# Optimization experiments

Hardware: AMD Instinct MI355X
Metric: run time of the kernel (lower is better)

## Reference

```python
import jax, jax.numpy as jnp
import numpy as np

PAA_SIZE = 64  # init_kwargs paa_size
GAF_TYPE = 'GADF'  # init_kwargs GAF_type


def setup_inputs() -> dict:
    key = jax.random.key(0)
    x = jax.random.uniform(key, (256, 4096, 32), dtype=jnp.float32)
    return {"x": x}


def reference(x):
    # x: [B, T, C]
    B, T, C = x.shape
    # --- rescale: per-sample, per-channel min-max over time axis -> [0, 1]
    x_min = jnp.min(x, axis=1, keepdims=True)
    x_max = jnp.max(x, axis=1, keepdims=True)
    r = (x - x_min) / (x_max - x_min)            # [B, T, C]
    # --- PAA: strided mean over bins of length size = T // paa_size
    size = T // PAA_SIZE
    p = r[:, : PAA_SIZE * size].reshape(B, PAA_SIZE, size, C).sum(axis=2) / size  # [B, P, C]
    # --- GAF construction
    y = jnp.sqrt(1.0 - p * p)                    # [B, P, C]
    if GAF_TYPE == 'GASF':
        # out[b,i,j,c] = x_i x_j - y_i y_j (symmetric)
        out = jnp.einsum('bic,bjc->bijc', p, p) - jnp.einsum('bic,bjc->bijc', y, y)
    else:  # 'GADF'
        # original: -transpose(y x^T - x y^T) => out[b,i,j,c] = y_i x_j - x_i y_j
        out = jnp.einsum('bic,bjc->bijc', y, p) - jnp.einsum('bic,bjc->bijc', p, y)
    return out  # [B, paa_size, paa_size, C]
```

## Files before the change

kernel.cpp:

```cpp
#include <hip/hip_runtime.h>
#include <math.h>

#define BB   256
#define TT   4096
#define CC   32
#define PP   64
#define PSTR 33

__device__ __forceinline__ float4 f4min(float4 a, float4 b) {
    return make_float4(fminf(a.x,b.x), fminf(a.y,b.y), fminf(a.z,b.z), fminf(a.w,b.w));
}
__device__ __forceinline__ float4 f4max(float4 a, float4 b) {
    return make_float4(fmaxf(a.x,b.x), fmaxf(a.y,b.y), fmaxf(a.z,b.z), fmaxf(a.w,b.w));
}
__device__ __forceinline__ void f4add(float4& a, float4 v) {
    a.x += v.x; a.y += v.y; a.z += v.z; a.w += v.w;
}
__device__ __forceinline__ float4 shflxor4(float4 v, int m) {
    return make_float4(__shfl_xor(v.x, m), __shfl_xor(v.y, m),
                       __shfl_xor(v.z, m), __shfl_xor(v.w, m));
}

__global__ __launch_bounds__(1024, 4) void gaf_kernel(const float* __restrict__ x,
                                                      float* __restrict__ out) {
    __shared__ float sp[PP * PSTR];
    __shared__ float sy[PP * PSTR];
    __shared__ float redmin[16 * CC];
    __shared__ float redmax[16 * CC];

    const int tid  = threadIdx.x;
    const int lane = tid & 63;
    const int wave = tid >> 6;
    const int cg   = lane & 7;
    const int b    = blockIdx.x;

    const float4* xw = (const float4*)x + (size_t)b * (TT * CC / 4) + wave * 2048 + lane;

    const float FBIG = 3.402823466e+38f;
    float4 mn = make_float4(FBIG, FBIG, FBIG, FBIG);
    float4 mx = make_float4(-FBIG, -FBIG, -FBIG, -FBIG);
    float4 acc[4];
    #pragma unroll
    for (int g = 0; g < 4; ++g) acc[g] = make_float4(0.f, 0.f, 0.f, 0.f);

    #pragma unroll
    for (int g = 0; g < 4; ++g) {
        float4 buf[8];
        #pragma unroll
        for (int u = 0; u < 8; ++u) buf[u] = xw[(g * 8 + u) * 64];
        #pragma unroll
        for (int u = 0; u < 8; ++u) {
            mn = f4min(mn, buf[u]); mx = f4max(mx, buf[u]); f4add(acc[g], buf[u]);
        }
    }

    #pragma unroll
    for (int m = 8; m <= 32; m <<= 1) {
        mn = f4min(mn, shflxor4(mn, m));
        mx = f4max(mx, shflxor4(mx, m));
        #pragma unroll
        for (int g = 0; g < 4; ++g) f4add(acc[g], shflxor4(acc[g], m));
    }

    if (lane < 8) {
        *(float4*)&redmin[wave * CC + cg * 4] = mn;
        *(float4*)&redmax[wave * CC + cg * 4] = mx;
    }
    __syncthreads();

    float4 gmn = *(const float4*)&redmin[0 * CC + cg * 4];
    float4 gmx = *(const float4*)&redmax[0 * CC + cg * 4];
    #pragma unroll
    for (int w = 1; w < 16; ++w) {
        gmn = f4min(gmn, *(const float4*)&redmin[w * CC + cg * 4]);
        gmx = f4max(gmx, *(const float4*)&redmax[w * CC + cg * 4]);
    }

    float4 inv;
    inv.x = 1.0f / (gmx.x - gmn.x);  inv.y = 1.0f / (gmx.y - gmn.y);
    inv.z = 1.0f / (gmx.z - gmn.z);  inv.w = 1.0f / (gmx.w - gmn.w);
    const float s64 = 1.0f / 64.0f;

    if (lane < 8) {
        #pragma unroll
        for (int g = 0; g < 4; ++g) {
            float4 p, y;
            p.x = (acc[g].x * s64 - gmn.x) * inv.x;  p.y = (acc[g].y * s64 - gmn.y) * inv.y;
            p.z = (acc[g].z * s64 - gmn.z) * inv.z;  p.w = (acc[g].w * s64 - gmn.w) * inv.w;
            y.x = sqrtf(fmaxf(1.f - p.x * p.x, 0.f));  y.y = sqrtf(fmaxf(1.f - p.y * p.y, 0.f));
            y.z = sqrtf(fmaxf(1.f - p.z * p.z, 0.f));  y.w = sqrtf(fmaxf(1.f - p.w * p.w, 0.f));
            const int s = wave * 4 + g;
            *(float4*)&sp[s * PSTR + cg * 4] = p;
            *(float4*)&sy[s * PSTR + cg * 4] = y;
        }
    }
    __syncthreads();

    const int jrow = lane >> 3;
    float4 pj[8], yj[8];
    #pragma unroll
    for (int jc = 0; jc < 8; ++jc) {
        const int j = jc * 8 + jrow;
        pj[jc] = *(const float4*)&sp[j * PSTR + cg * 4];
        yj[jc] = *(const float4*)&sy[j * PSTR + cg * 4];
    }

    float4* ob = (float4*)out + (size_t)b * (PP * PP * CC / 4) + wave * 2048 + lane;

    #pragma unroll
    for (int ii = 0; ii < 4; ++ii) {
        const int i = wave * 4 + ii;
        const float4 pi = *(const float4*)&sp[i * PSTR + cg * 4];
        const float4 yi = *(const float4*)&sy[i * PSTR + cg * 4];
        #pragma unroll
        for (int jc = 0; jc < 8; ++jc) {
            float4 r;
            r.x = yi.x * pj[jc].x - pi.x * yj[jc].x;
            r.y = yi.y * pj[jc].y - pi.y * yj[jc].y;
            r.z = yi.z * pj[jc].z - pi.z * yj[jc].z;
            r.w = yi.w * pj[jc].w - pi.w * yj[jc].w;
            ob[ii * 512 + jc * 64] = r;
        }
    }
}

extern "C" void kernel_launch(void* const* d_in, const int* in_sizes, int n_in,
                              void* d_out, int out_size, void* d_ws, size_t ws_size,
                              hipStream_t stream) {
    const float* x = (const float*)d_in[0];
    float* out = (float*)d_out;
    gaf_kernel<<<BB, 1024, 0, stream>>>(x, out);
}
```

Before: 231.0 us.

## Split GAF into stats and outer-product kernels with more blocks

Replaces the single 256-block fused kernel with two launches. The first computes per-segment sums and partial min/max across 2048 blocks and writes them to workspace. The second uses 1024 blocks to finish the reduction, build p/y, and write output with nontemporal stores. The aim is better occupancy of the GPU's compute units than one block per batch allows. The cost is a second launch and a small workspace round trip, and the old fused kernel is kept as a fallback when workspace is too small.

```diff
diff --git a/kernel.cpp b/kernel.cpp
--- a/kernel.cpp
+++ b/kernel.cpp
@@ -1,5 +1,6 @@
 #include <hip/hip_runtime.h>
 #include <math.h>
+
 
 #define BB   256
 #define TT   4096
@@ -7,6 +8,13 @@
 #define PP   64
 #define PSTR 33
 
+typedef float f32x4 __attribute__((ext_vector_type(4)));
+
+#define SEG_FLOATS  (BB * PP * CC)
+#define MM_FLOATS   (BB * 32 * CC)
+#define WS_FLOATS   (SEG_FLOATS + 2 * MM_FLOATS)
+#define WS_BYTES    (WS_FLOATS * 4)
+
 __device__ __forceinline__ float4 f4min(float4 a, float4 b) {
     return make_float4(fminf(a.x,b.x), fminf(a.y,b.y), fminf(a.z,b.z), fminf(a.w,b.w));
 }
@@ -20,9 +28,139 @@
     return make_float4(__shfl_xor(v.x, m), __shfl_xor(v.y, m),
                        __shfl_xor(v.z, m), __shfl_xor(v.w, m));
 }
-
-__global__ __launch_bounds__(1024, 4) void gaf_kernel(const float* __restrict__ x,
-                                                      float* __restrict__ out) {
+__device__ __forceinline__ void ntstore4(float4* dst, float4 v) {
+    f32x4 t; t.x = v.x; t.y = v.y; t.z = v.z; t.w = v.w;
+    __builtin_nontemporal_store(t, (f32x4*)dst);
+}
+
+__global__ __launch_bounds__(256, 8) void gaf_stats(const float* __restrict__ x,
+                                                    float* __restrict__ ws) {
+    const int tid  = threadIdx.x;
+    const int lane = tid & 63;
+    const int wave = tid >> 6;
+    const int cg   = lane & 7;
+    const int blk  = blockIdx.x;
+    const int b    = blk >> 3;
+    const int ch   = blk & 7;
+
+    const float4* base = (const float4*)x + (size_t)b * (TT * CC / 4)
+                         + ch * 4096 + wave * 1024 + lane;
+
+    const float FBIG = 3.402823466e+38f;
+    float4 mn = make_float4(FBIG, FBIG, FBIG, FBIG);
+    float4 mx = make_float4(-FBIG, -FBIG, -FBIG, -FBIG);
+    float4 acc0 = make_float4(0.f, 0.f, 0.f, 0.f);
+    float4 acc1 = make_float4(0.f, 0.f, 0.f, 0.f);
+
+    float4 buf[8];
+    #pragma unroll
+    for (int u = 0; u < 8; ++u) buf[u] = base[u * 64];
+    #pragma unroll
+    for (int u = 0; u < 8; ++u) { mn = f4min(mn, buf[u]); mx = f4max(mx, buf[u]); f4add(acc0, buf[u]); }
+    #pragma unroll
+    for (int u = 0; u < 8; ++u) buf[u] = base[(8 + u) * 64];
+    #pragma unroll
+    for (int u = 0; u < 8; ++u) { mn = f4min(mn, buf[u]); mx = f4max(mx, buf[u]); f4add(acc1, buf[u]); }
+
+    #pragma unroll
+    for (int m = 8; m <= 32; m <<= 1) {
+        mn = f4min(mn, shflxor4(mn, m));
+        mx = f4max(mx, shflxor4(mx, m));
+        f4add(acc0, shflxor4(acc0, m));
+        f4add(acc1, shflxor4(acc1, m));
+    }
+
+    if (lane < 8) {
+        const int s0 = ch * 8 + wave * 2;
+        *(float4*)&ws[(size_t)b * (PP * CC) + s0 * CC + cg * 4]       = acc0;
+        *(float4*)&ws[(size_t)b * (PP * CC) + (s0 + 1) * CC + cg * 4] = acc1;
+        const int k = ch * 4 + wave;
+        *(float4*)&ws[SEG_FLOATS             + (size_t)b * (32 * CC) + k * CC + cg * 4] = mn;
+        *(float4*)&ws[SEG_FLOATS + MM_FLOATS + (size_t)b * (32 * CC) + k * CC + cg * 4] = mx;
+    }
+}
+
+__global__ __launch_bounds__(256, 4) void gaf_outer(const float* __restrict__ ws,
+                                                    float* __restrict__ out) {
+    __shared__ float sp[PP * PSTR];
+    __shared__ float sy[PP * PSTR];
+    __shared__ float4 lmn[32];
+    __shared__ float4 lmx[32];
+
+    const int tid  = threadIdx.x;
+    const int lane = tid & 63;
+    const int wave = tid >> 6;
+    const int cg   = lane & 7;
+    const int blk  = blockIdx.x;
+    const int b    = blk >> 2;
+    const int i0   = (blk & 3) * 16;
+
+    {
+        const int k = wave * 8 + (lane >> 3);
+        float4 mnk = *(const float4*)&ws[SEG_FLOATS             + (size_t)b * (32 * CC) + k * CC + cg * 4];
+        float4 mxk = *(const float4*)&ws[SEG_FLOATS + MM_FLOATS + (size_t)b * (32 * CC) + k * CC + cg * 4];
+        #pragma unroll
+        for (int m = 8; m <= 32; m <<= 1) {
+            mnk = f4min(mnk, shflxor4(mnk, m));
+            mxk = f4max(mxk, shflxor4(mxk, m));
+        }
+        if (lane < 8) { lmn[wave * 8 + cg] = mnk; lmx[wave * 8 + cg] = mxk; }
+    }
+    __syncthreads();
+
+    {
+        const int cq = tid & 7;
+        float4 mnf = f4min(f4min(lmn[cq], lmn[8 + cq]), f4min(lmn[16 + cq], lmn[24 + cq]));
+        float4 mxf = f4max(f4max(lmx[cq], lmx[8 + cq]), f4max(lmx[16 + cq], lmx[24 + cq]));
+        float4 inv;
+        inv.x = 1.0f / (mxf.x - mnf.x);  inv.y = 1.0f / (mxf.y - mnf.y);
+        inv.z = 1.0f / (mxf.z - mnf.z);  inv.w = 1.0f / (mxf.w - mnf.w);
+        const float s64 = 1.0f / 64.0f;
+        #pragma unroll
+        for (int h = 0; h < 2; ++h) {
+            const int s = (tid >> 3) + h * 32;
+            float4 sum = *(const float4*)&ws[(size_t)b * (PP * CC) + s * CC + cq * 4];
+            float4 p, y;
+            p.x = (sum.x * s64 - mnf.x) * inv.x;  p.y = (sum.y * s64 - mnf.y) * inv.y;
+            p.z = (sum.z * s64 - mnf.z) * inv.z;  p.w = (sum.w * s64 - mnf.w) * inv.w;
+            y.x = sqrtf(fmaxf(1.f - p.x * p.x, 0.f));  y.y = sqrtf(fmaxf(1.f - p.y * p.y, 0.f));
+            y.z = sqrtf(fmaxf(1.f - p.z * p.z, 0.f));  y.w = sqrtf(fmaxf(1.f - p.w * p.w, 0.f));
+            *(float4*)&sp[s * PSTR + cq * 4] = p;
+            *(float4*)&sy[s * PSTR + cq * 4] = y;
+        }
+    }
+    __syncthreads();
+
+    const int jrow = lane >> 3;
+    float4 pj[8], yj[8];
+    #pragma unroll
+    for (int jc = 0; jc < 8; ++jc) {
+        const int j = jc * 8 + jrow;
+        pj[jc] = *(const float4*)&sp[j * PSTR + cg * 4];
+        yj[jc] = *(const float4*)&sy[j * PSTR + cg * 4];
+    }
+
+    float4* ob = (float4*)out + (size_t)b * (PP * PP * CC / 4) + lane;
+
+    #pragma unroll
+    for (int ii = 0; ii < 4; ++ii) {
+        const int i = i0 + wave * 4 + ii;
+        const float4 pi = *(const float4*)&sp[i * PSTR + cg * 4];
+        const float4 yi = *(const float4*)&sy[i * PSTR + cg * 4];
+        #pragma unroll
+        for (int jc = 0; jc < 8; ++jc) {
+            float4 r;
+            r.x = yi.x * pj[jc].x - pi.x * yj[jc].x;
+            r.y = yi.y * pj[jc].y - pi.y * yj[jc].y;
+            r.z = yi.z * pj[jc].z - pi.z * yj[jc].z;
+            r.w = yi.w * pj[jc].w - pi.w * yj[jc].w;
+            ntstore4(&ob[i * 512 + jc * 64], r);
+        }
+    }
+}
+
+__global__ __launch_bounds__(1024, 4) void gaf_fused(const float* __restrict__ x,
+                                                     float* __restrict__ out) {
     __shared__ float sp[PP * PSTR];
     __shared__ float sy[PP * PSTR];
     __shared__ float redmin[16 * CC];
@@ -109,9 +247,8 @@
 
     #pragma unroll
     for (int ii = 0; ii < 4; ++ii) {
-        const int i = wave * 4 + ii;
-        const float4 pi = *(const float4*)&sp[i * PSTR + cg * 4];
-        const float4 yi = *(const float4*)&sy[i * PSTR + cg * 4];
+        const float4 pi = *(const float4*)&sp[(wave * 4 + ii) * PSTR + cg * 4];
+        const float4 yi = *(const float4*)&sy[(wave * 4 + ii) * PSTR + cg * 4];
         #pragma unroll
         for (int jc = 0; jc < 8; ++jc) {
             float4 r;
@@ -129,5 +266,11 @@
                               hipStream_t stream) {
     const float* x = (const float*)d_in[0];
     float* out = (float*)d_out;
-    gaf_kernel<<<BB, 1024, 0, stream>>>(x, out);
-}
+    if (d_ws != nullptr && ws_size >= (size_t)WS_BYTES) {
+        float* ws = (float*)d_ws;
+        gaf_stats<<<BB * 8, 256, 0, stream>>>(x, ws);
+        gaf_outer<<<BB * 4, 256, 0, stream>>>(ws, out);
+    } else {
+        gaf_fused<<<BB, 1024, 0, stream>>>(x, out);
+    }
+}
```

Result: no change. 231.5 us (+0.2%).
